# Kernel tuning notes

Hardware: AMD Instinct MI355X
Metric: run time of the kernel (lower is better)

Reference implementation:

```python
import math
import jax, jax.numpy as jnp
import numpy as np


def setup_inputs() -> dict:
    key = jax.random.key(0)
    ks = jax.random.split(key, 6)
    B, L, d_model = 8, 4096, 512
    s = 1.0 / math.sqrt(d_model)
    inp = {
        "x": jax.random.normal(ks[0], (B, L, d_model), dtype=jnp.float32),
        "Wq": jax.random.normal(ks[1], (d_model, d_model), dtype=jnp.float32) * s,
        "bq": jnp.zeros((d_model,), jnp.float32),
        "Wk": jax.random.normal(ks[2], (d_model, d_model), dtype=jnp.float32) * s,
        "bk": jnp.zeros((d_model,), jnp.float32),
        "Wv": jax.random.normal(ks[3], (d_model, d_model), dtype=jnp.float32) * s,
        "bv": jnp.zeros((d_model,), jnp.float32),
        "Wo": jax.random.normal(ks[4], (d_model, d_model), dtype=jnp.float32) * s,
        "bo": jnp.zeros((d_model,), jnp.float32),
    }
    return inp


N_HEADS = 8
FACTOR = 1


def reference(x, Wq, bq, Wk, bk, Wv, bv, Wo, bo):
    B, L, d_model = x.shape
    H = N_HEADS
    D = d_model // H
    # projections (torch Linear: x @ W.T + b), reshape to (B,H,L,D)
    def proj(W, b):
        y = jnp.einsum("bld,ed->ble", x, W) + b
        return y.reshape(B, L, H, D).transpose(0, 2, 1, 3)
    q = proj(Wq, bq)
    k = proj(Wk, bk)
    v = proj(Wv, bv)
    # FFT autocorrelation along time axis (axis=2)
    q_f = jnp.fft.rfft(q, axis=2)
    k_f = jnp.fft.rfft(k, axis=2)
    corr = jnp.fft.irfft(q_f * jnp.conj(k_f), n=L, axis=2)  # (B,H,L,D)
    k_top = max(1, int(FACTOR * math.log(L + 1)))
    k_top = min(k_top, L)
    corr_mean = corr.mean(axis=-1)  # (B,H,L)
    top_vals, top_idx = jax.lax.top_k(corr_mean, k_top)  # (B,H,k)
    weights = jax.nn.softmax(top_vals, axis=-1)  # (B,H,k)
    t = jnp.arange(L).reshape(1, 1, 1, L)
    idx = (t + top_idx[..., None]) % L  # (B,H,k,L)
    # gather rolled V per selected lag: (B,H,k,L,D)
    v_exp = jnp.broadcast_to(v[:, :, None], (B, H, k_top, L, D))
    gathered = jnp.take_along_axis(v_exp, idx[..., None], axis=3)
    out = jnp.einsum("bhkld,bhk->bhld", gathered, weights)
    out = out.transpose(0, 2, 1, 3).reshape(B, L, d_model)
    # dropout=0.0 (eval): identity
    return jnp.einsum("bld,ed->ble", out, Wo) + bo
```

## Files before the change

kernel.cpp:

```cpp
#include <hip/hip_runtime.h>
#include <cstdint>
#include <cstddef>

#define AS1 __attribute__((address_space(1)))
#define AS3 __attribute__((address_space(3)))

using half8  = __attribute__((ext_vector_type(8))) _Float16;
using half4v = __attribute__((ext_vector_type(4))) _Float16;
using half2v = __attribute__((ext_vector_type(2))) _Float16;
using f32x4  = __attribute__((ext_vector_type(4))) float;

__global__ void prep_all_kernel(const float* __restrict__ x,
                                const float* __restrict__ Wq, const float* __restrict__ Wk,
                                const float* __restrict__ Wv, const float* __restrict__ Wo,
                                const float* __restrict__ bq, const float* __restrict__ bk,
                                const float* __restrict__ bv,
                                _Float16* __restrict__ xh, _Float16* __restrict__ Bt,
                                _Float16* __restrict__ WoH,
                                float2* __restrict__ tw, float* __restrict__ bias) {
    const int bid = blockIdx.x;
    const int tid = threadIdx.x;
    if (bid < 16384) {
        int i = (bid * 256 + tid) * 4;
        float4 v = *(const float4*)(x + i);
        half4v h;
        h[0] = (_Float16)v.x; h[1] = (_Float16)v.y;
        h[2] = (_Float16)v.z; h[3] = (_Float16)v.w;
        *(half4v*)(xh + i) = h;
    } else if (bid < 19456) {
        int i = (bid - 16384) * 256 + tid;
        int e = i >> 9, k = i & 511;
        int proj = e >> 9, er = e & 511;
        const float* W = (proj == 0) ? Wq : ((proj == 1) ? Wk : Wv);
        Bt[i] = (_Float16)W[er * 512 + k];
    } else if (bid < 20480) {
        int i = (bid - 19456) * 256 + tid;
        WoH[i] = (_Float16)Wo[i];
    } else if (bid < 20496) {
        int p = (bid - 20480) * 256 + tid;
        double th = -2.0 * 3.14159265358979323846 * (double)p / 4096.0;
        tw[p] = make_float2((float)cos(th), (float)sin(th));
    } else {
        int i = (bid - 20496) * 256 + tid;
        bias[i] = (i < 512) ? bq[i] : ((i < 1024) ? bk[i - 512] : bv[i - 1024]);
    }
}

template <int MODE>
__global__ __launch_bounds__(512, 2) void gemm_f16_kernel(
    const _Float16* __restrict__ A, const _Float16* __restrict__ Bt,
    const float* __restrict__ bias,
    _Float16* __restrict__ qT, _Float16* __restrict__ kT,
    _Float16* __restrict__ vout, float* __restrict__ Cout)
{
    constexpr int NBLK   = (MODE == 0) ? 6 : 2;
    constexpr int PERXCD = (MODE == 0) ? 96 : 32;
    __shared__ _Float16 smem[65536];

    const int gi = (blockIdx.x & 7) * PERXCD + (blockIdx.x >> 3);
    const int mb = gi / NBLK;
    const int nb = gi - mb * NBLK;
    const int m0 = mb * 256, n0 = nb * 256;
    const int tid = threadIdx.x;
    const int wave = tid >> 6, lane = tid & 63;
    const int lane15 = lane & 15, quad = lane >> 4;
    const int wmr = (wave >> 2) * 128;
    const int wnr = (wave & 3) * 64;

    const int row0 = tid >> 2;
    const int kq   = (tid & 3) ^ ((tid >> 3) & 3);
    const char* gA0 = (const char*)A  + ((size_t)(m0 + row0)) * 1024 + kq * 16;
    const char* gA1 = gA0 + (size_t)128 * 1024;
    const char* gB0 = (const char*)Bt + ((size_t)(n0 + row0)) * 1024 + kq * 16;
    const char* gB1 = gB0 + (size_t)128 * 1024;
    const int ldsA0 = wave * 1024;
    const int ldsA1 = 8192 + wave * 1024;
    const int ldsB0 = 16384 + wave * 1024;
    const int ldsB1 = 24576 + wave * 1024;

    const int coloff = ((quad ^ ((lane15 >> 1) & 3)) << 4);

    f32x4 acc[8][4];
#pragma unroll
    for (int mi = 0; mi < 8; mi++)
#pragma unroll
        for (int ni = 0; ni < 4; ni++)
#pragma unroll
            for (int r = 0; r < 4; r++) acc[mi][ni][r] = 0.f;

    auto STAGE = [&](int slot, int kt) {
        const int off = kt * 64;
        char* base = (char*)smem + slot * 32768;
        __builtin_amdgcn_global_load_lds((const AS1 void*)(gA0 + off), (AS3 void*)(base + ldsA0), 16, 0, 0);
        __builtin_amdgcn_global_load_lds((const AS1 void*)(gA1 + off), (AS3 void*)(base + ldsA1), 16, 0, 0);
        __builtin_amdgcn_global_load_lds((const AS1 void*)(gB0 + off), (AS3 void*)(base + ldsB0), 16, 0, 0);
        __builtin_amdgcn_global_load_lds((const AS1 void*)(gB1 + off), (AS3 void*)(base + ldsB1), 16, 0, 0);
    };
    auto COMPUTE = [&](int slot) {
        const char* ba = (const char*)smem + slot * 32768;
        const char* bb = ba + 16384;
        half8 af[8], bf[4];
#pragma unroll
        for (int mi = 0; mi < 8; mi++)
            af[mi] = *(const half8*)(ba + (wmr + mi * 16 + lane15) * 64 + coloff);
#pragma unroll
        for (int ni = 0; ni < 4; ni++)
            bf[ni] = *(const half8*)(bb + (wnr + ni * 16 + lane15) * 64 + coloff);
        __builtin_amdgcn_s_setprio(1);
#pragma unroll
        for (int mi = 0; mi < 8; mi++)
#pragma unroll
            for (int ni = 0; ni < 4; ni++)
                acc[mi][ni] = __builtin_amdgcn_mfma_f32_16x16x32_f16(af[mi], bf[ni], acc[mi][ni], 0, 0, 0);
        __builtin_amdgcn_s_setprio(0);
    };

    STAGE(0, 0); STAGE(1, 1); STAGE(2, 2);
    for (int t = 0; t <= 12; ++t) {
        STAGE((t + 3) & 3, t + 3);
        asm volatile("s_waitcnt vmcnt(12)" ::: "memory");
        __builtin_amdgcn_s_barrier();
        asm volatile("" ::: "memory");
        COMPUTE(t & 3);
        __builtin_amdgcn_s_barrier();
    }
    asm volatile("s_waitcnt vmcnt(8)" ::: "memory");
    __builtin_amdgcn_s_barrier();
    asm volatile("" ::: "memory");
    COMPUTE(1);
    __builtin_amdgcn_s_barrier();
    asm volatile("s_waitcnt vmcnt(4)" ::: "memory");
    __builtin_amdgcn_s_barrier();
    asm volatile("" ::: "memory");
    COMPUTE(2);
    __builtin_amdgcn_s_barrier();
    asm volatile("s_waitcnt vmcnt(0)" ::: "memory");
    __builtin_amdgcn_s_barrier();
    asm volatile("" ::: "memory");
    COMPUTE(3);

    if (MODE == 1) {
#pragma unroll
        for (int mi = 0; mi < 8; mi++)
#pragma unroll
            for (int ni = 0; ni < 4; ni++) {
                const int n = n0 + wnr + ni * 16 + lane15;
                const float bb = bias[n];
#pragma unroll
                for (int r = 0; r < 4; r++) {
                    const int m = m0 + wmr + mi * 16 + quad * 4 + r;
                    Cout[(size_t)m * 512 + n] = acc[mi][ni][r] + bb;
                }
            }
        return;
    }
    const int proj = n0 >> 9;
    if (proj == 2) {
#pragma unroll
        for (int mi = 0; mi < 8; mi++)
#pragma unroll
            for (int ni = 0; ni < 4; ni++) {
                const int n = n0 + wnr + ni * 16 + lane15;
                const int er = n - 1024, h = er >> 6, d = er & 63;
                const float bb = bias[n];
#pragma unroll
                for (int r = 0; r < 4; r++) {
                    const int m = m0 + wmr + mi * 16 + quad * 4 + r;
                    const int b = m >> 12, l = m & 4095;
                    vout[((size_t)((b * 8 + h) * 4096 + l)) * 64 + d] = (_Float16)(acc[mi][ni][r] + bb);
                }
            }
        return;
    }
    _Float16* dst = (proj == 0) ? qT : kT;
    const int b = m0 >> 12;
    const int lbase = (m0 & 4095) + wmr + quad * 4;
#pragma unroll
    for (int mi = 0; mi < 8; mi++)
#pragma unroll
        for (int ni = 0; ni < 4; ni++) {
            const int e = n0 + wnr + ni * 16 + lane15;
            const int er = e & 511, h = er >> 6, d = er & 63;
            const float bb = bias[e];
            half4v o;
            o[0] = (_Float16)(acc[mi][ni][0] + bb);
            o[1] = (_Float16)(acc[mi][ni][1] + bb);
            o[2] = (_Float16)(acc[mi][ni][2] + bb);
            o[3] = (_Float16)(acc[mi][ni][3] + bb);
            *(half4v*)(dst + ((size_t)((b * 8 + h) * 64 + d)) * 4096 + lbase + mi * 16) = o;
        }
}

__device__ __forceinline__ float2 cmul(float2 a, float2 b) {
    return make_float2(a.x * b.x - a.y * b.y, a.x * b.y + a.y * b.x);
}
__device__ __forceinline__ float2 cmulc(float2 a, float cr, float ci) {
    return make_float2(a.x * cr - a.y * ci, a.x * ci + a.y * cr);
}
__device__ __forceinline__ int swz(int i) { return i ^ ((i >> 4) & 15); }

__device__ __forceinline__ void dft16(float2 x[16]) {
    constexpr float wc[10] = {1.f, 0.92387953f, 0.70710678f, 0.38268343f, 0.f,
                              0.f, -0.70710678f, 0.f, 0.f, -0.92387953f};
    constexpr float wsn[10] = {0.f, -0.38268343f, -0.70710678f, -0.92387953f, -1.f,
                               0.f, -0.70710678f, 0.f, 0.f, 0.38268343f};
    float2 t[16];
#pragma unroll
    for (int u = 0; u < 4; u++) {
        const float2 a = x[u], b = x[u + 4], c = x[u + 8], d = x[u + 12];
        const float2 Ea = make_float2(a.x + c.x, a.y + c.y);
        const float2 Oa = make_float2(a.x - c.x, a.y - c.y);
        const float2 Eb = make_float2(b.x + d.x, b.y + d.y);
        const float2 Ob = make_float2(b.x - d.x, b.y - d.y);
        const float2 y0 = make_float2(Ea.x + Eb.x, Ea.y + Eb.y);
        const float2 y1 = make_float2(Oa.x + Ob.y, Oa.y - Ob.x);
        const float2 y2 = make_float2(Ea.x - Eb.x, Ea.y - Eb.y);
        const float2 y3 = make_float2(Oa.x - Ob.y, Oa.y + Ob.x);
        t[4 * u + 0] = y0;
        t[4 * u + 1] = cmulc(y1, wc[u * 1], wsn[u * 1]);
        t[4 * u + 2] = cmulc(y2, wc[u * 2], wsn[u * 2]);
        t[4 * u + 3] = cmulc(y3, wc[u * 3], wsn[u * 3]);
    }
#pragma unroll
    for (int v = 0; v < 4; v++) {
        const float2 a = t[v], b = t[v + 4], c = t[v + 8], d = t[v + 12];
        const float2 Ea = make_float2(a.x + c.x, a.y + c.y);
        const float2 Oa = make_float2(a.x - c.x, a.y - c.y);
        const float2 Eb = make_float2(b.x + d.x, b.y + d.y);
        const float2 Ob = make_float2(b.x - d.x, b.y - d.y);
        x[v]      = make_float2(Ea.x + Eb.x, Ea.y + Eb.y);
        x[v + 4]  = make_float2(Oa.x + Ob.y, Oa.y - Ob.x);
        x[v + 8]  = make_float2(Ea.x - Eb.x, Ea.y - Eb.y);
        x[v + 12] = make_float2(Oa.x - Ob.y, Oa.y + Ob.x);
    }
}

__device__ __forceinline__ void fft4096_r16(float2* buf, const float2* __restrict__ tw,
                                            int tid, float2 (&x)[16]) {
    __syncthreads();
#pragma unroll
    for (int j = 0; j < 16; j++) x[j] = buf[swz(tid + 256 * j)];
    __syncthreads();
    dft16(x);
    buf[swz(16 * tid)] = x[0];
#pragma unroll
    for (int m = 1; m < 16; m++) buf[swz(16 * tid + m)] = cmul(x[m], tw[tid * m]);
    __syncthreads();
#pragma unroll
    for (int j = 0; j < 16; j++) x[j] = buf[swz(tid + 256 * j)];
    __syncthreads();
    dft16(x);
    {
        const int q = tid & 15, p = tid >> 4;
        const int base = q + 256 * p;
        buf[swz(base)] = x[0];
#pragma unroll
        for (int m = 1; m < 16; m++)
            buf[swz(base + 16 * m)] = cmul(x[m], tw[(p * m) << 4]);
    }
    __syncthreads();
#pragma unroll
    for (int j = 0; j < 16; j++) x[j] = buf[swz(tid + 256 * j)];
    __syncthreads();
    dft16(x);
#pragma unroll
    for (int m = 0; m < 16; m++) buf[swz(tid + 256 * m)] = x[m];
    __syncthreads();
}

__global__ __launch_bounds__(256) void fft_partial_kernel(
    const _Float16* __restrict__ qT, const _Float16* __restrict__ kT,
    const float2* __restrict__ tw, float2* __restrict__ spec)
{
    __shared__ float2 buf[4096];
    const int tid = threadIdx.x;
    const int bh = blockIdx.x >> 4, chunk = blockIdx.x & 15;
    float sx[16], sy[16];
#pragma unroll
    for (int i = 0; i < 16; i++) { sx[i] = 0.f; sy[i] = 0.f; }
    const _Float16* qb = qT + (size_t)bh * 64 * 4096;
    const _Float16* kb = kT + (size_t)bh * 64 * 4096;
    float2 x[16];
    for (int dd = 0; dd < 4; dd++) {
        const int d = chunk * 4 + dd;
#pragma unroll
        for (int i = 0; i < 2; i++) {
            const int t0 = 2048 * i + tid * 8;
            const half8 fq = *(const half8*)(qb + d * 4096 + t0);
            const half8 fk = *(const half8*)(kb + d * 4096 + t0);
#pragma unroll
            for (int j = 0; j < 8; j++)
                buf[swz(t0 + j)] = make_float2((float)fq[j], (float)fk[j]);
        }
        fft4096_r16(buf, tw, tid, x);
#pragma unroll
        for (int i = 0; i < 16; i++) {
            const int f = tid + 256 * i;
            const float2 Zf = x[i];
            const float2 Zm = buf[swz((4096 - f) & 4095)];
            const float Qr  = 0.5f * (Zf.x + Zm.x);
            const float Qi  = 0.5f * (Zf.y - Zm.y);
            const float cKr = 0.5f * (Zf.y + Zm.y);
            const float cKi = 0.5f * (Zf.x - Zm.x);
            sx[i] += Qr * cKr - Qi * cKi;
            sy[i] += Qr * cKi + Qi * cKr;
        }
        __syncthreads();
    }
    float2* out = spec + (size_t)blockIdx.x * 4096;
#pragma unroll
    for (int i = 0; i < 16; i++) out[tid + 256 * i] = make_float2(sx[i], sy[i]);
}

__global__ __launch_bounds__(256) void sum_spec_kernel(
    const float4* __restrict__ spec4, float4* __restrict__ ssum4)
{
    const int bh = blockIdx.x >> 3;
    const int i4 = (blockIdx.x & 7) * 256 + threadIdx.x;
    const float4* base = spec4 + (size_t)bh * 16 * 2048 + i4;
    float4 s = make_float4(0.f, 0.f, 0.f, 0.f);
#pragma unroll
    for (int c = 0; c < 16; c++) {
        const float4 v = base[(size_t)c * 2048];
        s.x += v.x; s.y += v.y; s.z += v.z; s.w += v.w;
    }
    s.y = -s.y; s.w = -s.w;
    ssum4[(size_t)bh * 2048 + i4] = s;
}

__global__ __launch_bounds__(256) void reduce_topk_kernel(
    const float2* __restrict__ ssum, const float2* __restrict__ tw,
    int* __restrict__ top_idx, float* __restrict__ top_w)
{
    __shared__ float2 buf[4096];
    __shared__ float wv[4];
    __shared__ int wi[4];
    const int tid = threadIdx.x;
    const int bh = blockIdx.x;
#pragma unroll
    for (int i = 0; i < 16; i++) {
        const int f = tid + 256 * i;
        buf[swz(f)] = ssum[(size_t)bh * 4096 + f];
    }
    float2 x[16];
    fft4096_r16(buf, tw, tid, x);
    float vals[8]; int idxs[8];
    for (int k = 0; k < 8; k++) {
        float best = -3.0e38f; int bi = 0;
#pragma unroll
        for (int i = 0; i < 16; i++) {
            const int f = tid + 256 * i;
            const float c = buf[swz(f)].x;
            if (c > best) { best = c; bi = f; }
        }
#pragma unroll
        for (int off = 32; off > 0; off >>= 1) {
            const float ov = __shfl_down(best, off);
            const int oi = __shfl_down(bi, off);
            if (ov > best || (ov == best && oi < bi)) { best = ov; bi = oi; }
        }
        if ((tid & 63) == 0) { wv[tid >> 6] = best; wi[tid >> 6] = bi; }
        __syncthreads();
        if (tid == 0) {
            best = wv[0]; bi = wi[0];
            for (int w = 1; w < 4; w++) {
                if (wv[w] > best || (wv[w] == best && wi[w] < bi)) { best = wv[w]; bi = wi[w]; }
            }
            vals[k] = best; idxs[k] = bi;
            buf[swz(bi)].x = -3.4e38f;
        }
        __syncthreads();
    }
    if (tid == 0) {
        const float scale = 1.f / (4096.f * 64.f);
        float e[8], s = 0.f;
        const float mx = vals[0] * scale;
        for (int k = 0; k < 8; k++) { e[k] = __expf(vals[k] * scale - mx); s += e[k]; }
        for (int k = 0; k < 8; k++) {
            top_w[bh * 8 + k] = e[k] / s;
            top_idx[bh * 8 + k] = idxs[k];
        }
    }
}

__global__ __launch_bounds__(256) void gather_kernel(
    const half8* __restrict__ v8, const int* __restrict__ top_idx,
    const float* __restrict__ top_w, half8* __restrict__ out8)
{
    const int seq = blockIdx.x;
    const int bh = seq >> 7;
    const int lgrp = seq & 127;
    const int b = bh >> 3, h = bh & 7;
    const int tid = threadIdx.x;
    const int l = lgrp * 32 + (tid >> 3);
    const int d8 = tid & 7;
    int idx[8]; float w[8];
#pragma unroll
    for (int k = 0; k < 8; k++) { idx[k] = top_idx[bh * 8 + k]; w[k] = top_w[bh * 8 + k]; }
    const half8* vb = v8 + (size_t)bh * 4096 * 8;
    float a[8];
#pragma unroll
    for (int j = 0; j < 8; j++) a[j] = 0.f;
#pragma unroll
    for (int k = 0; k < 8; k++) {
        const int ls = (l + idx[k]) & 4095;
        const half8 pv = vb[(size_t)ls * 8 + d8];
#pragma unroll
        for (int j = 0; j < 8; j++) a[j] += w[k] * (float)pv[j];
    }
    half8 o;
#pragma unroll
    for (int j = 0; j < 8; j++) o[j] = (_Float16)a[j];
    out8[((size_t)(b * 4096 + l)) * 64 + h * 8 + d8] = o;
}

extern "C" void kernel_launch(void* const* d_in, const int* in_sizes, int n_in,
                              void* d_out, int out_size, void* d_ws, size_t ws_size,
                              hipStream_t stream) {
    (void)in_sizes; (void)n_in; (void)out_size; (void)ws_size;
    const float* x  = (const float*)d_in[0];
    const float* Wq = (const float*)d_in[1];
    const float* bq = (const float*)d_in[2];
    const float* Wk = (const float*)d_in[3];
    const float* bk = (const float*)d_in[4];
    const float* Wv = (const float*)d_in[5];
    const float* bv = (const float*)d_in[6];
    const float* Wo = (const float*)d_in[7];
    const float* bo = (const float*)d_in[8];
    float* out = (float*)d_out;

    char* ws = (char*)d_ws;
    size_t off = 0;
    auto alloc = [&](size_t bytes) -> void* {
        void* p = ws + off; off += (bytes + 255) & ~(size_t)255; return p;
    };
    _Float16* xh   = (_Float16*)alloc(33554432);
    _Float16* qT   = (_Float16*)alloc(33554432);
    _Float16* kT   = (_Float16*)alloc(33554432);
    _Float16* vbuf = (_Float16*)alloc(33554432);
    float2* spec   = (float2*)alloc(33554432);
    float2* ssum   = (float2*)alloc(2097152);
    _Float16* BtH  = (_Float16*)alloc(1572864);
    _Float16* WoH  = (_Float16*)alloc(524288);
    float* biasQKV = (float*)alloc(6144);
    float2* tw     = (float2*)alloc(32768);
    int*   top_idx = (int*)alloc(2048);
    float* top_w   = (float*)alloc(2048);
    _Float16* out_pre = xh;

    prep_all_kernel<<<20502, 256, 0, stream>>>(x, Wq, Wk, Wv, Wo, bq, bk, bv,
                                               xh, BtH, WoH, tw, biasQKV);
    gemm_f16_kernel<0><<<768, 512, 0, stream>>>(xh, BtH, biasQKV, qT, kT, vbuf, nullptr);
    fft_partial_kernel<<<1024, 256, 0, stream>>>(qT, kT, tw, spec);
    sum_spec_kernel<<<512, 256, 0, stream>>>((const float4*)spec, (float4*)ssum);
    reduce_topk_kernel<<<64, 256, 0, stream>>>(ssum, tw, top_idx, top_w);
    gather_kernel<<<8192, 256, 0, stream>>>((const half8*)vbuf, top_idx, top_w,
                                            (half8*)out_pre);
    gemm_f16_kernel<1><<<256, 512, 0, stream>>>(out_pre, WoH, bo, nullptr, nullptr, nullptr, out);
}
```

Before: 319.6 us.

## Restructure GEMM main loop into interleaved half-tile ping-pong pipeline

Rewrites the GEMM K-loop from a 4-slot, 64-wide K staging scheme to a 2-slot, 128-wide K tile split into two 64-wide sub-tiles. LDS fragment loads, async global-to-LDS staging and MFMA batches are interleaved in half-M chunks with finer barriers. The goal is better overlap of memory traffic with matrix math and lower register pressure, since only 4 A fragments are held at a time. The gather kernel also remaps block indices so neighbouring sequence groups land on the same XCD for L2 locality. The added barriers and tighter wait counts risk extra sync stalls.

Result: faster. 310.7 us (median of 2 runs) (-2.8%).

```diff
diff --git a/kernel.cpp b/kernel.cpp
--- a/kernel.cpp
+++ b/kernel.cpp
@@ -67,18 +67,12 @@
     const int wmr = (wave >> 2) * 128;
     const int wnr = (wave & 3) * 64;
 
-    const int row0 = tid >> 2;
-    const int kq   = (tid & 3) ^ ((tid >> 3) & 3);
-    const char* gA0 = (const char*)A  + ((size_t)(m0 + row0)) * 1024 + kq * 16;
-    const char* gA1 = gA0 + (size_t)128 * 1024;
-    const char* gB0 = (const char*)Bt + ((size_t)(n0 + row0)) * 1024 + kq * 16;
-    const char* gB1 = gB0 + (size_t)128 * 1024;
-    const int ldsA0 = wave * 1024;
-    const int ldsA1 = 8192 + wave * 1024;
-    const int ldsB0 = 16384 + wave * 1024;
-    const int ldsB1 = 24576 + wave * 1024;
-
-    const int coloff = ((quad ^ ((lane15 >> 1) & 3)) << 4);
+    const int r0 = tid >> 2;
+    const int c0 = (tid & 3) ^ ((tid >> 3) & 3);
+    const char* gA = (const char*)A  + ((size_t)(m0 + r0)) * 1024 + c0 * 16;
+    const char* gB = (const char*)Bt + ((size_t)(n0 + r0)) * 1024 + c0 * 16;
+    const int sbw = wave * 1024;
+    const int coloff = (quad ^ ((lane15 >> 1) & 3)) << 4;
 
     f32x4 acc[8][4];
 #pragma unroll
@@ -88,56 +82,79 @@
 #pragma unroll
             for (int r = 0; r < 4; r++) acc[mi][ni][r] = 0.f;
 
-    auto STAGE = [&](int slot, int kt) {
-        const int off = kt * 64;
-        char* base = (char*)smem + slot * 32768;
-        __builtin_amdgcn_global_load_lds((const AS1 void*)(gA0 + off), (AS3 void*)(base + ldsA0), 16, 0, 0);
-        __builtin_amdgcn_global_load_lds((const AS1 void*)(gA1 + off), (AS3 void*)(base + ldsA1), 16, 0, 0);
-        __builtin_amdgcn_global_load_lds((const AS1 void*)(gB0 + off), (AS3 void*)(base + ldsB0), 16, 0, 0);
-        __builtin_amdgcn_global_load_lds((const AS1 void*)(gB1 + off), (AS3 void*)(base + ldsB1), 16, 0, 0);
+    auto STAGE = [&](int slot, int tensor, int kk, int kt) {
+        const char* g = (tensor == 0 ? gA : gB) + kt * 128 + kk * 64;
+        char* base = (char*)smem + slot * 65536 + tensor * 32768 + kk * 16384 + sbw;
+        __builtin_amdgcn_global_load_lds((const AS1 void*)g, (AS3 void*)base, 16, 0, 0);
+        __builtin_amdgcn_global_load_lds((const AS1 void*)(g + 131072), (AS3 void*)(base + 8192), 16, 0, 0);
     };
-    auto COMPUTE = [&](int slot) {
-        const char* ba = (const char*)smem + slot * 32768;
-        const char* bb = ba + 16384;
-        half8 af[8], bf[4];
-#pragma unroll
-        for (int mi = 0; mi < 8; mi++)
-            af[mi] = *(const half8*)(ba + (wmr + mi * 16 + lane15) * 64 + coloff);
-#pragma unroll
-        for (int ni = 0; ni < 4; ni++)
-            bf[ni] = *(const half8*)(bb + (wnr + ni * 16 + lane15) * 64 + coloff);
+
+    half8 af[4], bf[4];
+    auto LOADA = [&](int slot, int kk, int mh) {
+        const char* ba = (const char*)smem + slot * 65536 + kk * 16384;
+#pragma unroll
+        for (int j = 0; j < 4; j++)
+            af[j] = *(const half8*)(ba + (wmr + (mh * 4 + j) * 16 + lane15) * 64 + coloff);
+    };
+    auto LOADB = [&](int slot, int kk) {
+        const char* bb = (const char*)smem + slot * 65536 + 32768 + kk * 16384;
+#pragma unroll
+        for (int j = 0; j < 4; j++)
+            bf[j] = *(const half8*)(bb + (wnr + j * 16 + lane15) * 64 + coloff);
+    };
+    auto MMA = [&](int mh) {
         __builtin_amdgcn_s_setprio(1);
 #pragma unroll
-        for (int mi = 0; mi < 8; mi++)
+        for (int j = 0; j < 4; j++)
 #pragma unroll
             for (int ni = 0; ni < 4; ni++)
-                acc[mi][ni] = __builtin_amdgcn_mfma_f32_16x16x32_f16(af[mi], bf[ni], acc[mi][ni], 0, 0, 0);
+                acc[mh * 4 + j][ni] =
+                    __builtin_amdgcn_mfma_f32_16x16x32_f16(af[j], bf[ni], acc[mh * 4 + j][ni], 0, 0, 0);
         __builtin_amdgcn_s_setprio(0);
     };
-
-    STAGE(0, 0); STAGE(1, 1); STAGE(2, 2);
-    for (int t = 0; t <= 12; ++t) {
-        STAGE((t + 3) & 3, t + 3);
-        asm volatile("s_waitcnt vmcnt(12)" ::: "memory");
-        __builtin_amdgcn_s_barrier();
-        asm volatile("" ::: "memory");
-        COMPUTE(t & 3);
-        __builtin_amdgcn_s_barrier();
-    }
-    asm volatile("s_waitcnt vmcnt(8)" ::: "memory");
-    __builtin_amdgcn_s_barrier();
-    asm volatile("" ::: "memory");
-    COMPUTE(1);
-    __builtin_amdgcn_s_barrier();
-    asm volatile("s_waitcnt vmcnt(4)" ::: "memory");
-    __builtin_amdgcn_s_barrier();
-    asm volatile("" ::: "memory");
-    COMPUTE(2);
-    __builtin_amdgcn_s_barrier();
-    asm volatile("s_waitcnt vmcnt(0)" ::: "memory");
-    __builtin_amdgcn_s_barrier();
-    asm volatile("" ::: "memory");
-    COMPUTE(3);
+#define BAR() do { __builtin_amdgcn_s_barrier(); asm volatile("" ::: "memory"); } while (0)
+#define VMW(n) asm volatile("s_waitcnt vmcnt(" #n ")" ::: "memory")
+
+    STAGE(0, 0, 0, 0); STAGE(0, 1, 0, 0);
+    STAGE(0, 0, 1, 0); STAGE(0, 1, 1, 0);
+    STAGE(1, 0, 0, 1); STAGE(1, 1, 0, 1);
+    VMW(8);
+    BAR();
+
+    for (int t = 0; t < 6; ++t) {
+        const int slot = t & 1, nslot = slot ^ 1;
+        LOADA(slot, 0, 0); LOADB(slot, 0);
+        STAGE(nslot, 0, 1, t + 1);
+        BAR(); MMA(0); BAR();
+        LOADA(slot, 0, 1);
+        STAGE(nslot, 1, 1, t + 1);
+        BAR(); MMA(1);
+        VMW(8);
+        BAR();
+        LOADA(slot, 1, 0); LOADB(slot, 1);
+        STAGE(slot, 0, 0, t + 2);
+        BAR(); MMA(0); BAR();
+        LOADA(slot, 1, 1);
+        STAGE(slot, 1, 0, t + 2);
+        BAR(); MMA(1);
+        VMW(8);
+        BAR();
+    }
+    LOADA(0, 0, 0); LOADB(0, 0); STAGE(1, 0, 1, 7); BAR(); MMA(0); BAR();
+    LOADA(0, 0, 1);              STAGE(1, 1, 1, 7); BAR(); MMA(1);
+    VMW(8); BAR();
+    LOADA(0, 1, 0); LOADB(0, 1); BAR(); MMA(0); BAR();
+    LOADA(0, 1, 1);              BAR(); MMA(1);
+    VMW(4);
+    BAR();
+    LOADA(1, 0, 0); LOADB(1, 0); BAR(); MMA(0); BAR();
+    LOADA(1, 0, 1);              BAR(); MMA(1);
+    VMW(0);
+    BAR();
+    LOADA(1, 1, 0); LOADB(1, 1); BAR(); MMA(0); BAR();
+    LOADA(1, 1, 1);              BAR(); MMA(1);
+#undef BAR
+#undef VMW
 
     if (MODE == 1) {
 #pragma unroll
@@ -387,9 +404,9 @@
     const half8* __restrict__ v8, const int* __restrict__ top_idx,
     const float* __restrict__ top_w, half8* __restrict__ out8)
 {
-    const int seq = blockIdx.x;
-    const int bh = seq >> 7;
-    const int lgrp = seq & 127;
+    const int gi = (blockIdx.x & 7) * 1024 + (blockIdx.x >> 3);
+    const int bh = gi >> 7;
+    const int lgrp = gi & 127;
     const int b = bh >> 3, h = bh & 7;
     const int tid = threadIdx.x;
     const int l = lgrp * 32 + (tid >> 3);
```
